# Kernel tuning notes

Measured on AMD Instinct MI355X. Metric: run time of the kernel, lower is better.

The kernel has to match this reference:

```python
import jax, jax.numpy as jnp
import numpy as np

# ---- static lookup-point config (matches cfg.radius/stride/level) ----
RADIUS = [4, 4, 4, 4]
STRIDE = [1, 1, 1, 1]
LEVEL = [0, 1, 2, 3]

def _build_pts():
    pts = {}
    for r, s, l in zip(RADIUS, STRIDE, LEVEL):
        pts.setdefault(l, set())
        for x in range(-r, r + 1):
            for y in range(-r, r + 1):
                pts[l].add((x * s, y * s))
    # sorted() reproduces torch's `v.sort()` on (x, y) tuples
    return {l: np.array(sorted(v), dtype=np.float32) for l, v in sorted(pts.items())}

PTS = _build_pts()                       # {lvl: (n_lvl, 2) offsets in level pixels}
N_LEVELS = max(LEVEL) + 1                # 4
CORR_DIM = 2 * sum(len(v) for v in PTS.values())   # 648
C_HALF = CORR_DIM // 2                   # 324 = per-direction channels
B, C, H, W = 1, 256, 80, 80


def _bilinear_sample(corr, x, y):
    """corr: (B, P, h, w); x, y: (P, n) pixel coords (align_corners=False convention,
    already converted to pixel space). Zero padding outside. Returns (B, P, n)."""
    Bn, P, h, w = corr.shape
    cf = corr.reshape(Bn, P, h * w)
    x0 = jnp.floor(x)
    y0 = jnp.floor(y)
    wx1 = x - x0
    wy1 = y - y0
    x0i = x0.astype(jnp.int32)
    y0i = y0.astype(jnp.int32)
    out = jnp.zeros((Bn, P, x.shape[-1]), corr.dtype)
    for dx, wxx in ((0, 1.0 - wx1), (1, wx1)):
        for dy, wyy in ((0, 1.0 - wy1), (1, wy1)):
            xi = x0i + dx
            yi = y0i + dy
            valid = (xi >= 0) & (xi < w) & (yi >= 0) & (yi < h)
            idx = jnp.clip(yi, 0, h - 1) * w + jnp.clip(xi, 0, w - 1)   # (P, n)
            v = jnp.take_along_axis(cf, jnp.broadcast_to(idx[None], (Bn,) + idx.shape), axis=2)
            out = out + v * (wxx * wyy * valid)[None]
    return out


def _lookup_pyramid(pyr):
    """pyr[lvl]: (B, P, H>>lvl, W>>lvl). Returns (B, P, C_HALF)."""
    outs = []
    for lvl, pts in PTS.items():
        s = 1 << lvl
        n = pts.shape[0]
        dxy = jnp.asarray(pts)
        # grid_sample align_corners=False: level-pixel coord of full-res pixel j is
        # (2j+1)/(2s) - 0.5; neighbor offsets are exactly `pts` in level pixels.
        bx = (2.0 * jnp.arange(W) + 1.0) / (2.0 * s) - 0.5   # (W,)
        by = (2.0 * jnp.arange(H) + 1.0) / (2.0 * s) - 0.5   # (H,)
        x = jnp.broadcast_to(bx[None, :, None] + dxy[None, None, :, 0], (H, W, n)).reshape(H * W, n)
        y = jnp.broadcast_to(by[:, None, None] + dxy[None, None, :, 1], (H, W, n)).reshape(H * W, n)
        outs.append(_bilinear_sample(pyr[lvl], x, y))
    return jnp.concatenate(outs, axis=-1)


def _pyramid(corr):
    """corr: (B, P, H, W) -> list of avg-pooled levels (2x2, stride 2)."""
    p = [corr]
    for _ in range(N_LEVELS - 1):
        b, pp, h, w = corr.shape
        corr = corr.reshape(b, pp, h // 2, 2, w // 2, 2).mean(axis=(3, 5))
        p.append(corr)
    return p


def _conv3x3_relu(x, w, b):
    y = jax.lax.conv_general_dilated(x, w, (1, 1), 'SAME',
                                     dimension_numbers=('NHWC', 'HWIO', 'NHWC'))
    return jax.nn.relu(y + b)


def _layer_norm(x, g, b, eps=1e-5):
    m = x.mean(-1, keepdims=True)
    v = ((x - m) ** 2).mean(-1, keepdims=True)
    return (x - m) * jax.lax.rsqrt(v + eps) * g + b


def setup_inputs() -> dict:
    key = jax.random.key(0)
    ks = jax.random.split(key, 4)
    return {
        'f0': jax.random.normal(ks[0], (B, C, H, W), jnp.float32),
        'f1': jax.random.normal(ks[1], (B, C, H, W), jnp.float32),
        'conv_w1': jax.random.normal(ks[2], (3, 3, C_HALF, C_HALF), jnp.float32) * 0.02,
        'conv_b1': jnp.zeros((C_HALF,), jnp.float32),
        'conv_w2': jax.random.normal(ks[3], (3, 3, C_HALF, C_HALF), jnp.float32) * 0.02,
        'conv_b2': jnp.zeros((C_HALF,), jnp.float32),
        'ln_g': jnp.ones((C_HALF,), jnp.float32),
        'ln_b': jnp.zeros((C_HALF,), jnp.float32),
    }


def reference(f0, f1, conv_w1, conv_b1, conv_w2, conv_b2, ln_g, ln_b):
    Bn, Cn, Hn, Wn = f0.shape
    P = Hn * Wn
    a = f0.reshape(Bn, Cn, P)
    bb = f1.reshape(Bn, Cn, P)
    corr01 = jnp.einsum('bcp,bcq->bpq', a, bb)          # (B, P, P)
    corr10 = jnp.swapaxes(corr01, 1, 2)
    feat01 = _lookup_pyramid(_pyramid(corr01.reshape(Bn, P, Hn, Wn)))   # (B, P, C_HALF)
    feat10 = _lookup_pyramid(_pyramid(corr10.reshape(Bn, P, Hn, Wn)))

    def branch(feat):
        x = feat.reshape(Bn, Hn, Wn, C_HALF)
        y = x + _conv3x3_relu(_conv3x3_relu(x, conv_w1, conv_b1), conv_w2, conv_b2)
        y = _layer_norm(y, ln_g, ln_b)
        return jnp.transpose(y, (0, 3, 1, 2))           # (B, C_HALF, H, W)

    return jnp.concatenate([branch(feat01), branch(feat10)], axis=1)    # (B, 2*C_HALF, H, W)
```

## Files before the change

kernel.cpp:

```cpp
#include <hip/hip_runtime.h>

typedef unsigned short u16;
typedef unsigned int   u32;
typedef float f32x4 __attribute__((ext_vector_type(4)));
typedef __bf16 bf16x8 __attribute__((ext_vector_type(8)));
typedef unsigned short u16x8 __attribute__((ext_vector_type(8)));

#define PP   6400
#define HH   80
#define WW   80
#define KC   256
#define CH   324
#define CPAD 384
#define PW   82
#define PPIX (PW*PW)
#define NPOOL 2176

__device__ inline float b2f(u16 u) { union { u32 i; float f; } v; v.i = ((u32)u) << 16; return v.f; }
__device__ inline u16 f2b(float f) {
    union { u32 i; float f; } v; v.f = f;
    u32 r = v.i + 0x7fffu + ((v.i >> 16) & 1u);
    return (u16)(r >> 16);
}

__device__ __forceinline__ void gload16(const void* g, void* l) {
    __builtin_amdgcn_global_load_lds((const __attribute__((address_space(1))) void*)g,
                                     (__attribute__((address_space(3))) void*)l, 16, 0, 0);
}

__global__ __launch_bounds__(256) void prep_f(const float* __restrict__ f0,
                                              const float* __restrict__ f1,
                                              u16* __restrict__ fA, u16* __restrict__ fB) {
    __shared__ float tile[64][65];
    int p0 = blockIdx.x * 64, c0 = blockIdx.y * 64;
    const float* src = blockIdx.z ? f1 : f0;
    u16* dst = blockIdx.z ? fB : fA;
    int tid = threadIdx.x;
#pragma unroll
    for (int it = 0; it < 16; ++it) {
        int idx = tid + it * 256;
        int cc = idx >> 6, pp = idx & 63;
        tile[cc][pp] = src[(size_t)(c0 + cc) * PP + p0 + pp];
    }
    __syncthreads();
#pragma unroll
    for (int it = 0; it < 16; ++it) {
        int idx = tid + it * 256;
        int pp = idx >> 6, cc = idx & 63;
        dst[(size_t)(p0 + pp) * KC + c0 + cc] = f2b(tile[cc][pp]);
    }
}

__global__ __launch_bounds__(256) void prep_w(const float* __restrict__ w1,
                                              const float* __restrict__ w2,
                                              u16* __restrict__ wT1, u16* __restrict__ wT2) {
    __shared__ float tile[64][65];
    int tap = blockIdx.x;
    int t6 = blockIdx.y;
    int ci0 = (t6 / 6) * 64, co0 = (t6 % 6) * 64;
    const float* w = blockIdx.z ? w2 : w1;
    u16* wT = blockIdx.z ? wT2 : wT1;
    int tid = threadIdx.x;
#pragma unroll
    for (int it = 0; it < 16; ++it) {
        int idx = tid + it * 256;
        int ciL = idx >> 6, coL = idx & 63;
        int ci = ci0 + ciL, co = co0 + coL;
        tile[ciL][coL] = (ci < CH && co < CH) ? w[((size_t)tap * CH + ci) * CH + co] : 0.f;
    }
    __syncthreads();
#pragma unroll
    for (int it = 0; it < 16; ++it) {
        int idx = tid + it * 256;
        int coL = idx >> 6, ciL = idx & 63;
        wT[((size_t)tap * CPAD + co0 + coL) * CPAD + ci0 + ciL] = f2b(tile[ciL][coL]);
    }
}

__global__ __launch_bounds__(384) void prep_b(const float* __restrict__ b1,
                                              const float* __restrict__ b2,
                                              float* __restrict__ b1p, float* __restrict__ b2p) {
    int t = threadIdx.x;
    b1p[t] = t < CH ? b1[t] : 0.f;
    b2p[t] = t < CH ? b2[t] : 0.f;
}

__global__ __launch_bounds__(384) void zero_border(u16* __restrict__ feat, u16* __restrict__ t1) {
    int bi = blockIdx.x, dir = blockIdx.y;
    int pix;
    if (bi < 82) pix = bi;
    else if (bi < 164) pix = 81 * PW + (bi - 82);
    else if (bi < 244) pix = (bi - 164 + 1) * PW;
    else pix = (bi - 244 + 1) * PW + 81;
    size_t off = ((size_t)dir * PPIX + pix) * CPAD + threadIdx.x;
    feat[off] = 0;
    t1[off] = 0;
}

__global__ __launch_bounds__(256) void pool_feat(const u16* __restrict__ fA,
                                                 const u16* __restrict__ fB,
                                                 u16* __restrict__ pbarA,
                                                 u16* __restrict__ pbarB) {
    int j = blockIdx.x;
    const u16* src = blockIdx.y ? fA : fB;
    u16* dst = blockIdx.y ? pbarA : pbarB;
    int k = threadIdx.x;
    int cy3 = j / 10, cx3 = j % 10;
    float l1v[16], l2v[4];
#pragma unroll
    for (int a = 0; a < 4; ++a)
#pragma unroll
        for (int b = 0; b < 4; ++b) {
            int cy = cy3 * 4 + a, cx = cx3 * 4 + b;
            int p00 = (2 * cy) * 80 + 2 * cx;
            float v = 0.25f * (b2f(src[(size_t)p00 * KC + k]) + b2f(src[(size_t)(p00 + 1) * KC + k]) +
                               b2f(src[(size_t)(p00 + 80) * KC + k]) + b2f(src[(size_t)(p00 + 81) * KC + k]));
            l1v[a * 4 + b] = v;
            dst[(size_t)(cy * 40 + cx) * KC + k] = f2b(v);
        }
#pragma unroll
    for (int a = 0; a < 2; ++a)
#pragma unroll
        for (int b = 0; b < 2; ++b) {
            float v = 0.25f * (l1v[(2 * a) * 4 + 2 * b] + l1v[(2 * a) * 4 + 2 * b + 1] +
                               l1v[(2 * a + 1) * 4 + 2 * b] + l1v[(2 * a + 1) * 4 + 2 * b + 1]);
            l2v[a * 2 + b] = v;
            dst[(size_t)(1600 + (cy3 * 2 + a) * 20 + cx3 * 2 + b) * KC + k] = f2b(v);
        }
    float v3 = 0.25f * (l2v[0] + l2v[1] + l2v[2] + l2v[3]);
    dst[(size_t)(2000 + j) * KC + k] = f2b(v3);
}

__global__ __launch_bounds__(256) void gemm_cp(const u16* __restrict__ fA,
                                               const u16* __restrict__ fB,
                                               const u16* __restrict__ pbarA,
                                               const u16* __restrict__ pbarB,
                                               u16* __restrict__ corr01,
                                               u16* __restrict__ corr10,
                                               u16* __restrict__ pc) {
    int y = blockIdx.y, z = blockIdx.z;
    bool band = (y < 7);
    int m0 = blockIdx.x * 128, n0;
    const u16 *Aptr, *Bptr;
    if (band) {
        if (z) return;
        int n0t = (int)blockIdx.x + y - 3;
        if (n0t < 0 || n0t >= 50) return;
        n0 = n0t * 128;
        Aptr = fA; Bptr = fB;
    } else {
        n0 = (y - 7) * 128;
        Aptr = z ? fB : fA;
        Bptr = z ? pbarA : pbarB;
    }
    __shared__ __align__(16) char smem[128 * 136 * 2];
    u16* As = (u16*)smem;
    u16* Bs = As + 128 * 64;
    u16* trans = (u16*)smem;
    const int TS = 136;
    int tid = threadIdx.x;
    int wave = tid >> 6, lane = tid & 63;
    int quad = lane >> 4, l16 = lane & 15;
    int lrow = lane >> 3, lchunk = lane & 7;
    int sc = lchunk ^ (lrow & 7);
    int sw = l16 & 7;
    int wr = (wave >> 1) * 64, wc = (wave & 1) * 64;
    f32x4 acc[4][4] = {};

    for (int k0 = 0; k0 < KC; k0 += 64) {
        __syncthreads();
#pragma unroll
        for (int i = 0; i < 4; ++i) {
            int row = i * 32 + wave * 8 + lrow;
            gload16(&Aptr[(size_t)(m0 + row) * KC + k0 + sc * 8], &As[(i * 32 + wave * 8) * 64]);
            gload16(&Bptr[(size_t)(n0 + row) * KC + k0 + sc * 8], &Bs[(i * 32 + wave * 8) * 64]);
        }
        __syncthreads();
#pragma unroll
        for (int ki = 0; ki < 2; ++ki) {
            bf16x8 af[4], bfr[4];
#pragma unroll
            for (int mi = 0; mi < 4; ++mi) {
                int r = wr + mi * 16 + l16;
                af[mi] = *(const bf16x8*)(&As[r * 64 + (((ki * 4 + quad) ^ sw) * 8)]);
            }
#pragma unroll
            for (int ni = 0; ni < 4; ++ni) {
                int r = wc + ni * 16 + l16;
                bfr[ni] = *(const bf16x8*)(&Bs[r * 64 + (((ki * 4 + quad) ^ sw) * 8)]);
            }
#pragma unroll
            for (int mi = 0; mi < 4; ++mi)
#pragma unroll
                for (int ni = 0; ni < 4; ++ni)
                    acc[mi][ni] = __builtin_amdgcn_mfma_f32_16x16x32_bf16(af[mi], bfr[ni], acc[mi][ni], 0, 0, 0);
        }
    }
    if (!band) {
        int dir = z;
#pragma unroll
        for (int mi = 0; mi < 4; ++mi)
#pragma unroll
            for (int ni = 0; ni < 4; ++ni)
#pragma unroll
                for (int rr = 0; rr < 4; ++rr) {
                    int row = m0 + wr + mi * 16 + quad * 4 + rr;
                    int col = n0 + wc + ni * 16 + l16;
                    pc[((size_t)dir * PP + row) * NPOOL + col] = f2b(acc[mi][ni][rr]);
                }
        return;
    }
#pragma unroll
    for (int mi = 0; mi < 4; ++mi)
#pragma unroll
        for (int ni = 0; ni < 4; ++ni)
#pragma unroll
            for (int rr = 0; rr < 4; ++rr) {
                int row = m0 + wr + mi * 16 + quad * 4 + rr;
                int col = n0 + wc + ni * 16 + l16;
                corr01[(size_t)row * PP + col] = f2b(acc[mi][ni][rr]);
            }
    __syncthreads();
#pragma unroll
    for (int mi = 0; mi < 4; ++mi)
#pragma unroll
        for (int ni = 0; ni < 4; ++ni) {
            int c = wc + ni * 16 + l16;
            int rbase = wr + mi * 16 + quad * 4;
#pragma unroll
            for (int h = 0; h < 2; ++h) {
                u32 pk = (u32)f2b(acc[mi][ni][2 * h]) | ((u32)f2b(acc[mi][ni][2 * h + 1]) << 16);
                *(u32*)(&trans[c * TS + rbase + 2 * h]) = pk;
            }
        }
    __syncthreads();
#pragma unroll
    for (int it = 0; it < 8; ++it) {
        int c = it * 16 + (tid >> 4);
        int r8 = (tid & 15) * 8;
        u16x8 v = *(const u16x8*)(&trans[c * TS + r8]);
        *(u16x8*)(&corr10[(size_t)(n0 + c) * PP + m0 + r8]) = v;
    }
}

__global__ __launch_bounds__(384) void lookup(const u16* __restrict__ corr01,
                                              const u16* __restrict__ corr10,
                                              const u16* __restrict__ pc,
                                              u16* __restrict__ feat) {
    __shared__ __align__(16) u16 pcrow[4][NPOOL];
    __shared__ float l0buf[4][81];
    int p0 = blockIdx.x * 4, dir = blockIdx.y;
    int tid = threadIdx.x;
    const u16* corr = dir ? corr10 : corr01;
    for (int i = tid; i < 4 * (NPOOL / 8); i += 384) {
        int j = i / (NPOOL / 8), cc = i % (NPOOL / 8);
        *(u16x8*)(&pcrow[j][cc * 8]) =
            *(const u16x8*)(&pc[((size_t)dir * PP + p0 + j) * NPOOL + cc * 8]);
    }
    if (tid < 324) {
        int j = tid / 81, i = tid % 81;
        int p = p0 + j;
        int px = p % WW, py = p / WW;
        int dx = i / 9 - 4, dy = i % 9 - 4;
        int x = px + dx, yy = py + dy;
        float v = 0.f;
        if ((unsigned)x < (unsigned)WW && (unsigned)yy < (unsigned)HH)
            v = b2f(corr[(size_t)p * PP + yy * WW + x]);
        l0buf[j][i] = v;
    }
    __syncthreads();
    int ch = tid;
#pragma unroll
    for (int j = 0; j < 4; ++j) {
        int p = p0 + j;
        int px = p % WW, py = p / WW;
        float val = 0.f;
        if (ch < CH) {
            int lvl = ch / 81, i = ch % 81;
            if (lvl == 0) {
                val = l0buf[j][i];
            } else {
                int dx = i / 9 - 4, dy = i % 9 - 4;
                int wl = WW >> lvl;
                int base = (lvl == 1) ? 0 : (lvl == 2) ? 1600 : 2000;
                float inv = 1.0f / (float)(2 << lvl);
                float xc = (float)(2 * px + 1) * inv - 0.5f + (float)dx;
                float yc = (float)(2 * py + 1) * inv - 0.5f + (float)dy;
                float x0f = floorf(xc), y0f = floorf(yc);
                int x0 = (int)x0f, y0 = (int)y0f;
                float wx = xc - x0f, wy = yc - y0f;
#pragma unroll
                for (int cy = 0; cy < 2; ++cy)
#pragma unroll
                    for (int cx = 0; cx < 2; ++cx) {
                        int xi = x0 + cx, yi = y0 + cy;
                        if ((unsigned)xi < (unsigned)wl && (unsigned)yi < (unsigned)wl) {
                            float wgt = (cx ? wx : 1.f - wx) * (cy ? wy : 1.f - wy);
                            val += b2f(pcrow[j][base + yi * wl + xi]) * wgt;
                        }
                    }
            }
        }
        size_t pix = (size_t)(py + 1) * PW + px + 1;
        feat[((size_t)dir * PPIX + pix) * CPAD + ch] = f2b(val);
    }
}

__global__ __launch_bounds__(256) void conv_gemm(const u16* __restrict__ inFeat,
                                                 const u16* __restrict__ wTt,
                                                 const float* __restrict__ bias,
                                                 const u16* __restrict__ resid,
                                                 u16* __restrict__ outb) {
    int L = (int)blockIdx.x;
    int xcd = L & 7;
    int q = L >> 3;
    int n_t = q % 3; q /= 3;
    int mg = q % 13;
    int dir = q / 13;
    int m_t = mg * 8 + xcd;
    if (m_t >= 100) return;
    const u16* Ain = inFeat + (size_t)dir * PPIX * CPAD;
    const u16* Rin = resid ? resid + (size_t)dir * PPIX * CPAD : (const u16*)0;
    u16* Out = outb + (size_t)dir * PPIX * CPAD;
    __shared__ __align__(16) u16 As[64 * 128];
    __shared__ __align__(16) u16 Bs[128 * 128];
    int tid = threadIdx.x;
    int wave = tid >> 6, lane = tid & 63;
    int quad = lane >> 4, l16 = lane & 15;
    int wr = (wave >> 1) * 32, wc = (wave & 1) * 64;
    int m0 = m_t * 64, n0 = n_t * 128;
    f32x4 acc[2][4] = {};

    int pixA[4], scI[4];
#pragma unroll
    for (int i = 0; i < 4; ++i) {
        int r = wave * 16 + i * 4 + quad;
        int m = m0 + r;
        pixA[i] = (m / 80 + 1) * PW + (m % 80) + 1;
        scI[i] = l16 ^ ((i * 4 + quad) & 15);
    }

    for (int tap = 0; tap < 9; ++tap) {
        int dpix = (tap / 3 - 1) * PW + (tap % 3) - 1;
        const u16* Wt = wTt + ((size_t)tap * CPAD + n0) * CPAD;
#pragma unroll
        for (int kt = 0; kt < 3; ++kt) {
            int kc = kt * 128;
            __syncthreads();
#pragma unroll
            for (int i = 0; i < 4; ++i)
                gload16(&Ain[(size_t)(pixA[i] + dpix) * CPAD + kc + scI[i] * 8],
                        &As[(wave * 16 + i * 4) * 128]);
#pragma unroll
            for (int j = 0; j < 8; ++j) {
                int rb = wave * 32 + j * 4;
                gload16(&Wt[(size_t)(rb + quad) * CPAD + kc + scI[j & 3] * 8],
                        &Bs[rb * 128]);
            }
            __syncthreads();
#pragma unroll
            for (int ki = 0; ki < 4; ++ki) {
                int slot = (ki * 4 + quad) ^ l16;
                bf16x8 af[2], bfr[4];
#pragma unroll
                for (int mi = 0; mi < 2; ++mi)
                    af[mi] = *(const bf16x8*)(&As[(wr + mi * 16 + l16) * 128 + slot * 8]);
#pragma unroll
                for (int ni = 0; ni < 4; ++ni)
                    bfr[ni] = *(const bf16x8*)(&Bs[(wc + ni * 16 + l16) * 128 + slot * 8]);
#pragma unroll
                for (int mi = 0; mi < 2; ++mi)
#pragma unroll
                    for (int ni = 0; ni < 4; ++ni)
                        acc[mi][ni] = __builtin_amdgcn_mfma_f32_16x16x32_bf16(af[mi], bfr[ni], acc[mi][ni], 0, 0, 0);
            }
        }
    }
#pragma unroll
    for (int mi = 0; mi < 2; ++mi)
#pragma unroll
        for (int rr = 0; rr < 4; ++rr) {
            int p = m0 + wr + mi * 16 + quad * 4 + rr;
            size_t opix = (size_t)(p / 80 + 1) * PW + (p % 80) + 1;
#pragma unroll
            for (int ni = 0; ni < 4; ++ni) {
                int co = n0 + wc + ni * 16 + l16;
                float v = acc[mi][ni][rr] + bias[co];
                v = fmaxf(v, 0.f);
                if (Rin) v += b2f(Rin[opix * CPAD + co]);
                Out[opix * CPAD + co] = f2b(v);
            }
        }
}

__global__ __launch_bounds__(256) void ln_out(const u16* __restrict__ t2,
                                              const float* __restrict__ g,
                                              const float* __restrict__ b,
                                              float* __restrict__ out) {
    int dir = blockIdx.y;
    int p0 = blockIdx.x * 64;
    const u16* Y = t2 + (size_t)dir * PPIX * CPAD;
    __shared__ u16 buf[64 * 325];
    __shared__ float mean_s[64], inv_s[64];
    __shared__ float part[64][4][2];
    int tid = threadIdx.x;
    for (int idx = tid; idx < 64 * CH; idx += 256) {
        int pp = idx / CH, c = idx - pp * CH;
        int p = p0 + pp;
        size_t pix = (size_t)(p / 80 + 1) * PW + (p % 80) + 1;
        buf[pp * 325 + c] = Y[pix * CPAD + c];
    }
    __syncthreads();
    {
        int pp = tid >> 2, q = tid & 3;
        float s = 0.f, s2 = 0.f;
        for (int c = q; c < CH; c += 4) { float v = b2f(buf[pp * 325 + c]); s += v; s2 += v * v; }
        part[pp][q][0] = s; part[pp][q][1] = s2;
    }
    __syncthreads();
    if (tid < 64) {
        float s = 0.f, s2 = 0.f;
        for (int q = 0; q < 4; ++q) { s += part[tid][q][0]; s2 += part[tid][q][1]; }
        float m = s / (float)CH;
        float var = s2 / (float)CH - m * m;
        if (var < 0.f) var = 0.f;
        mean_s[tid] = m;
        inv_s[tid] = rsqrtf(var + 1e-5f);
    }
    __syncthreads();
    for (int idx = tid; idx < CH * 64; idx += 256) {
        int c = idx >> 6, pp = idx & 63;
        float v = (b2f(buf[pp * 325 + c]) - mean_s[pp]) * inv_s[pp] * g[c] + b[c];
        out[((size_t)(dir * CH + c)) * PP + p0 + pp] = v;
    }
}

extern "C" void kernel_launch(void* const* d_in, const int* in_sizes, int n_in,
                              void* d_out, int out_size, void* d_ws, size_t ws_size,
                              hipStream_t stream) {
    const float* f0  = (const float*)d_in[0];
    const float* f1  = (const float*)d_in[1];
    const float* w1  = (const float*)d_in[2];
    const float* b1  = (const float*)d_in[3];
    const float* w2  = (const float*)d_in[4];
    const float* b2  = (const float*)d_in[5];
    const float* lng = (const float*)d_in[6];
    const float* lnb = (const float*)d_in[7];
    float* out = (float*)d_out;

    char* ws = (char*)d_ws;
    size_t off = 0;
    auto alloc = [&](size_t bytes) -> char* {
        char* r = ws + off;
        off += (bytes + 511) & ~(size_t)511;
        return r;
    };
    u16* fA     = (u16*)alloc((size_t)PP * KC * 2);
    u16* fB     = (u16*)alloc((size_t)PP * KC * 2);
    u16* corr01 = (u16*)alloc((size_t)PP * PP * 2);
    u16* corr10 = (u16*)alloc((size_t)PP * PP * 2);
    u16* pc     = (u16*)alloc((size_t)2 * PP * NPOOL * 2);
    u16* feat   = (u16*)alloc((size_t)2 * PPIX * CPAD * 2);
    u16* t1     = (u16*)alloc((size_t)2 * PPIX * CPAD * 2);
    u16* t2     = (u16*)alloc((size_t)2 * PPIX * CPAD * 2);
    u16* pbarA  = (u16*)alloc((size_t)NPOOL * KC * 2);
    u16* pbarB  = (u16*)alloc((size_t)NPOOL * KC * 2);
    u16* wT1    = (u16*)alloc((size_t)9 * CPAD * CPAD * 2);
    u16* wT2    = (u16*)alloc((size_t)9 * CPAD * CPAD * 2);
    float* b1p  = (float*)alloc(CPAD * 4);
    float* b2p  = (float*)alloc(CPAD * 4);

    prep_f<<<dim3(100, 4, 2), 256, 0, stream>>>(f0, f1, fA, fB);
    prep_w<<<dim3(9, 36, 2), 256, 0, stream>>>(w1, w2, wT1, wT2);
    prep_b<<<1, 384, 0, stream>>>(b1, b2, b1p, b2p);
    zero_border<<<dim3(324, 2), 384, 0, stream>>>(feat, t1);
    pool_feat<<<dim3(100, 2), 256, 0, stream>>>(fA, fB, pbarA, pbarB);
    gemm_cp<<<dim3(50, 24, 2), 256, 0, stream>>>(fA, fB, pbarA, pbarB, corr01, corr10, pc);
    lookup<<<dim3(1600, 2), 384, 0, stream>>>(corr01, corr10, pc, feat);
    conv_gemm<<<dim3(624), 256, 0, stream>>>(feat, wT1, b1p, (const u16*)0, t1);
    conv_gemm<<<dim3(624), 256, 0, stream>>>(t1, wT2, b2p, feat, t2);
    ln_out<<<dim3(100, 2), 256, 0, stream>>>(t2, lng, lnb, out);
}
```

Before: 277.0 us.

## Double-buffer conv GEMM LDS tiles with 64-wide K steps and prefetch

Restructures the implicit-GEMM 3x3 conv mainloop to use two LDS buffers with a K-step of 64. The next tap/K-slice is issued asynchronously before computing on the current one, with explicit vmcnt waits and raw barriers instead of __syncthreads. It also raises MFMA priority with s_setprio. The goal is to hide global-load latency behind MFMA work. In exchange it doubles the number of barrier iterations and depends on the hand-counted vmcnt being correct.

```diff
diff --git a/kernel.cpp b/kernel.cpp
--- a/kernel.cpp
+++ b/kernel.cpp
@@ -322,59 +322,74 @@
     const u16* Ain = inFeat + (size_t)dir * PPIX * CPAD;
     const u16* Rin = resid ? resid + (size_t)dir * PPIX * CPAD : (const u16*)0;
     u16* Out = outb + (size_t)dir * PPIX * CPAD;
-    __shared__ __align__(16) u16 As[64 * 128];
-    __shared__ __align__(16) u16 Bs[128 * 128];
+    __shared__ __align__(16) u16 As2[2][64 * 64];
+    __shared__ __align__(16) u16 Bs2[2][128 * 64];
     int tid = threadIdx.x;
     int wave = tid >> 6, lane = tid & 63;
     int quad = lane >> 4, l16 = lane & 15;
+    int lrow = lane >> 3, lchunk = lane & 7;
+    int sc = lchunk ^ lrow;
+    int sw = l16 & 7;
     int wr = (wave >> 1) * 32, wc = (wave & 1) * 64;
     int m0 = m_t * 64, n0 = n_t * 128;
     f32x4 acc[2][4] = {};
 
-    int pixA[4], scI[4];
-#pragma unroll
-    for (int i = 0; i < 4; ++i) {
-        int r = wave * 16 + i * 4 + quad;
-        int m = m0 + r;
+    int pixA[2];
+#pragma unroll
+    for (int i = 0; i < 2; ++i) {
+        int m = m0 + wave * 16 + i * 8 + lrow;
         pixA[i] = (m / 80 + 1) * PW + (m % 80) + 1;
-        scI[i] = l16 ^ ((i * 4 + quad) & 15);
-    }
-
-    for (int tap = 0; tap < 9; ++tap) {
+    }
+    size_t bRow[4];
+#pragma unroll
+    for (int j = 0; j < 4; ++j)
+        bRow[j] = (size_t)(n0 + wave * 32 + j * 8 + lrow) * CPAD;
+
+    auto STAGE = [&](int t, int buf) {
+        int tap = t / 6, kt = t - tap * 6;
+        int kc = kt * 64 + sc * 8;
         int dpix = (tap / 3 - 1) * PW + (tap % 3) - 1;
-        const u16* Wt = wTt + ((size_t)tap * CPAD + n0) * CPAD;
-#pragma unroll
-        for (int kt = 0; kt < 3; ++kt) {
-            int kc = kt * 128;
-            __syncthreads();
-#pragma unroll
-            for (int i = 0; i < 4; ++i)
-                gload16(&Ain[(size_t)(pixA[i] + dpix) * CPAD + kc + scI[i] * 8],
-                        &As[(wave * 16 + i * 4) * 128]);
-#pragma unroll
-            for (int j = 0; j < 8; ++j) {
-                int rb = wave * 32 + j * 4;
-                gload16(&Wt[(size_t)(rb + quad) * CPAD + kc + scI[j & 3] * 8],
-                        &Bs[rb * 128]);
-            }
-            __syncthreads();
-#pragma unroll
-            for (int ki = 0; ki < 4; ++ki) {
-                int slot = (ki * 4 + quad) ^ l16;
-                bf16x8 af[2], bfr[4];
-#pragma unroll
-                for (int mi = 0; mi < 2; ++mi)
-                    af[mi] = *(const bf16x8*)(&As[(wr + mi * 16 + l16) * 128 + slot * 8]);
+        const u16* Wt = wTt + (size_t)tap * CPAD * CPAD;
+        u16* Asb = &As2[buf][0];
+        u16* Bsb = &Bs2[buf][0];
+#pragma unroll
+        for (int i = 0; i < 2; ++i)
+            gload16(&Ain[(size_t)(pixA[i] + dpix) * CPAD + kc], &Asb[(wave * 16 + i * 8) * 64]);
+#pragma unroll
+        for (int j = 0; j < 4; ++j)
+            gload16(&Wt[bRow[j] + kc], &Bsb[(wave * 32 + j * 8) * 64]);
+    };
+
+    STAGE(0, 0);
+    for (int t = 0; t < 54; ++t) {
+        int cur = t & 1;
+        if (t < 53) {
+            STAGE(t + 1, cur ^ 1);
+            asm volatile("s_waitcnt vmcnt(6)" ::: "memory");
+        } else {
+            asm volatile("s_waitcnt vmcnt(0)" ::: "memory");
+        }
+        __builtin_amdgcn_s_barrier();
+        const u16* Asb = &As2[cur][0];
+        const u16* Bsb = &Bs2[cur][0];
+#pragma unroll
+        for (int ki = 0; ki < 2; ++ki) {
+            bf16x8 af[2], bfr[4];
+#pragma unroll
+            for (int mi = 0; mi < 2; ++mi)
+                af[mi] = *(const bf16x8*)(&Asb[(wr + mi * 16 + l16) * 64 + (((ki * 4 + quad) ^ sw) * 8)]);
+#pragma unroll
+            for (int ni = 0; ni < 4; ++ni)
+                bfr[ni] = *(const bf16x8*)(&Bsb[(wc + ni * 16 + l16) * 64 + (((ki * 4 + quad) ^ sw) * 8)]);
+            __builtin_amdgcn_s_setprio(1);
+#pragma unroll
+            for (int mi = 0; mi < 2; ++mi)
 #pragma unroll
                 for (int ni = 0; ni < 4; ++ni)
-                    bfr[ni] = *(const bf16x8*)(&Bs[(wc + ni * 16 + l16) * 128 + slot * 8]);
-#pragma unroll
-                for (int mi = 0; mi < 2; ++mi)
-#pragma unroll
-                    for (int ni = 0; ni < 4; ++ni)
-                        acc[mi][ni] = __builtin_amdgcn_mfma_f32_16x16x32_bf16(af[mi], bfr[ni], acc[mi][ni], 0, 0, 0);
-            }
-        }
+                    acc[mi][ni] = __builtin_amdgcn_mfma_f32_16x16x32_bf16(af[mi], bfr[ni], acc[mi][ni], 0, 0, 0);
+            __builtin_amdgcn_s_setprio(0);
+        }
+        __builtin_amdgcn_s_barrier();
     }
 #pragma unroll
     for (int mi = 0; mi < 2; ++mi)
```

After: 296.7 us. 1.07x slower.
